# Optimization experiments

Measured on AMD Instinct MI355X. Metric: run time of the kernel, lower is better.

The kernel has to match this reference:

```python
import jax, jax.numpy as jnp
import numpy as np

N = 100000
F = 128
H = 4
C = 32
E = 1600000
LEAKY_ALPHA = 0.2


def setup_inputs() -> dict:
    key = jax.random.key(0)
    k1, k2, k3, k4, k5 = jax.random.split(key, 5)
    x = jax.random.normal(k1, (N, F), dtype=jnp.float32)
    edge_index = jax.random.randint(k2, (E, 2), 0, N, dtype=jnp.int64)  # cols: (source, target)
    kernel = jax.random.normal(k3, (F, H, C), dtype=jnp.float32) * 0.05
    attn_kernel_self = jax.random.normal(k4, (C, H), dtype=jnp.float32) * 0.05
    attn_kernel_neighs = jax.random.normal(k5, (C, H), dtype=jnp.float32) * 0.05
    bias = jnp.zeros((H * C,), dtype=jnp.float32)
    return {"x": x, "edge_index": edge_index, "kernel": kernel,
            "attn_kernel_self": attn_kernel_self,
            "attn_kernel_neighs": attn_kernel_neighs, "bias": bias}


def _gat_forward(x, edge_index, kernel, attn_kernel_self, attn_kernel_neighs, bias):
    n = x.shape[0]
    # add self loops: append (i, i) for every node
    loops = jnp.arange(n, dtype=edge_index.dtype)
    indices = jnp.concatenate([edge_index, jnp.stack([loops, loops], axis=1)], axis=0)
    sources, targets = indices[:, 0], indices[:, 1]

    xp = jnp.einsum('nf,fhc->nhc', x, kernel)                 # [N,H,C]
    attn_self = jnp.einsum('nhc,ch->nh', xp, attn_kernel_self)    # [N,H]
    attn_neigh = jnp.einsum('nhc,ch->nh', xp, attn_kernel_neighs)  # [N,H]

    logits = attn_self[targets] + attn_neigh[sources]          # [Etot,H]
    logits = jnp.where(logits >= 0, logits, LEAKY_ALPHA * logits)  # leaky_relu(0.2)

    # segment softmax over targets (every node has a self loop -> no empty segments)
    seg_max = jax.ops.segment_max(logits, targets, num_segments=n)
    e = jnp.exp(logits - seg_max[targets])
    seg_sum = jax.ops.segment_sum(e, targets, num_segments=n)
    alpha = e / seg_sum[targets]                               # [Etot,H]

    # weighted aggregation (dropout is identity at inference)
    msgs = alpha[..., None] * xp[sources]                      # [Etot,H,C]
    out = jax.ops.segment_sum(msgs, targets, num_segments=n)   # [N,H,C]

    out = out.reshape(n, H * C) + bias                         # concat heads + bias, linear activation
    return out, alpha[..., None]


def reference(x, edge_index, kernel, attn_kernel_self, attn_kernel_neighs, bias):
    return _gat_forward(x, edge_index, kernel, attn_kernel_self, attn_kernel_neighs, bias)
```

## Files before the change

kernel.cpp:

```cpp
#include <hip/hip_runtime.h>
#include <hip/hip_bf16.h>
#include <math.h>

#define LEAKY(x) ((x) >= 0.0f ? (x) : 0.2f * (x))
#define CHUNK 8192

typedef __attribute__((ext_vector_type(8))) short short8;
typedef __attribute__((ext_vector_type(4))) float f32x4;
typedef __attribute__((ext_vector_type(2))) int i32x2;

__device__ __forceinline__ float bf_lo(uint32_t u) { return __uint_as_float(u << 16); }
__device__ __forceinline__ float bf_hi(uint32_t u) { return __uint_as_float(u & 0xffff0000u); }
__device__ __forceinline__ uint32_t pack2(float a, float b) {
    __hip_bfloat162 h = __float22bfloat162_rn(make_float2(a, b));
    return *reinterpret_cast<uint32_t*>(&h);
}

__global__ __launch_bounds__(256) void w_prep(
    const float* __restrict__ W, uint32_t* __restrict__ Wp)
{
    const int slot = blockIdx.x * 256 + threadIdx.x;
    if (slot >= 2048) return;
    const int kb = slot >> 9;
    const int cb = (slot >> 6) & 7;
    const int l  = slot & 63;
    const int k0 = kb * 32 + (l >> 4) * 8;
    const int col = cb * 16 + (l & 15);
    uint32_t u[4];
    #pragma unroll
    for (int p = 0; p < 4; ++p) {
        const float a = W[(size_t)(k0 + 2 * p) * 128 + col];
        const float b = W[(size_t)(k0 + 2 * p + 1) * 128 + col];
        u[p] = pack2(a, b);
    }
    *(uint4*)&Wp[(size_t)slot * 4] = make_uint4(u[0], u[1], u[2], u[3]);
}

__global__ __launch_bounds__(256) void gemm_xp(
    const float* __restrict__ x, const uint32_t* __restrict__ Wp,
    const float* __restrict__ aks, const float* __restrict__ akn,
    uint32_t* __restrict__ xpb, float* __restrict__ attn_self,
    float* __restrict__ attn_nei, int N)
{
    __shared__ float xs[64][133];
    const int t  = threadIdx.x;
    const int w  = t >> 6;
    const int l  = t & 63;
    const int nb = blockIdx.x * 64;

    const int row  = nb + w * 16 + (l & 15);
    const int rowc = min(row, N - 1);
    const int kg   = (l >> 4) * 8;
    const float* xrow = x + (size_t)rowc * 128 + kg;

    f32x4 acc[8] = {};
    #pragma unroll
    for (int kb = 0; kb < 4; ++kb) {
        const float4 x0 = *(const float4*)(xrow + kb * 32);
        const float4 x1 = *(const float4*)(xrow + kb * 32 + 4);
        union { short8 s; uint32_t u[4]; } A;
        A.u[0] = pack2(x0.x, x0.y); A.u[1] = pack2(x0.z, x0.w);
        A.u[2] = pack2(x1.x, x1.y); A.u[3] = pack2(x1.z, x1.w);
        #pragma unroll
        for (int cb = 0; cb < 8; ++cb) {
            union { short8 s; uint4 u; } B;
            B.u = *(const uint4*)&Wp[(((size_t)(kb * 8 + cb)) * 64 + l) * 4];
            acc[cb] = __builtin_amdgcn_mfma_f32_16x16x32_bf16(A.s, B.s, acc[cb], 0, 0, 0);
        }
    }

    const int r0 = (l >> 4) * 4;
    const int cl = l & 15;
    #pragma unroll
    for (int cb = 0; cb < 8; ++cb)
        #pragma unroll
        for (int r = 0; r < 4; ++r)
            xs[w * 16 + r0 + r][cb * 16 + cl] = acc[cb][r];
    __syncthreads();

    #pragma unroll
    for (int i = 0; i < 16; ++i) {
        const int idx = t + i * 256;
        const int n = idx >> 6, q = idx & 63;
        const int gn = nb + n;
        if (gn < N)
            xpb[(size_t)gn * 64 + q] = pack2(xs[n][2 * q], xs[n][2 * q + 1]);
    }

    {
        const int n = t & 63, h = t >> 6;
        const int gn = nb + n;
        if (gn < N) {
            float ss = 0.0f, sn = 0.0f;
            #pragma unroll
            for (int c = 0; c < 32; ++c) {
                const float v = xs[n][h * 32 + c];
                ss = fmaf(v, aks[c * 4 + h], ss);
                sn = fmaf(v, akn[c * 4 + h], sn);
            }
            attn_self[(size_t)gn * 4 + h] = ss;
            attn_nei [(size_t)gn * 4 + h] = sn;
        }
    }
}

__global__ __launch_bounds__(256) void binA(
    const int* __restrict__ ei, int2* __restrict__ stage,
    int* __restrict__ start_table, int* __restrict__ bucket_tot,
    int NB, int E)
{
    __shared__ int lh[512], lex[512], ss[256];
    const int t    = threadIdx.x;
    const int base = blockIdx.x * CHUNK;
    const int end  = min(E, base + CHUNK);

    for (int i = t; i < 512; i += 256) lh[i] = 0;
    __syncthreads();
    for (int i = base + t; i < end; i += 256)
        atomicAdd(&lh[((const int2*)ei)[i].y >> 8], 1);
    __syncthreads();

    const int v0 = lh[2 * t], v1 = lh[2 * t + 1];
    ss[t] = v0 + v1;
    __syncthreads();
    for (int d = 1; d < 256; d <<= 1) {
        const int add = (t >= d) ? ss[t - d] : 0;
        __syncthreads();
        ss[t] += add;
        __syncthreads();
    }
    const int ex = ss[t] - v0 - v1;
    lex[2 * t] = ex;
    lex[2 * t + 1] = ex + v0;
    __syncthreads();

    const size_t cbase = (size_t)blockIdx.x * (NB + 1);
    for (int b = t; b <= NB; b += 256) start_table[cbase + b] = base + lex[b];
    for (int b = t; b < NB; b += 256)
        if (lh[b]) atomicAdd(&bucket_tot[b], lh[b]);
    __syncthreads();

    for (int i = base + t; i < end; i += 256) {
        const int2 e2 = ((const int2*)ei)[i];
        const int slot = atomicAdd(&lex[e2.y >> 8], 1);
        stage[base + slot] = e2;
    }
}

__global__ __launch_bounds__(256) void bucket_scan(
    const int* __restrict__ bucket_tot, int* __restrict__ bucket_off,
    int* __restrict__ offsets, int NB, int N, int E)
{
    __shared__ int ss[256];
    const int t = threadIdx.x;
    const int v0 = (2 * t     < NB) ? bucket_tot[2 * t]     : 0;
    const int v1 = (2 * t + 1 < NB) ? bucket_tot[2 * t + 1] : 0;
    ss[t] = v0 + v1;
    __syncthreads();
    for (int d = 1; d < 256; d <<= 1) {
        const int add = (t >= d) ? ss[t - d] : 0;
        __syncthreads();
        ss[t] += add;
        __syncthreads();
    }
    const int ex = ss[t] - v0 - v1;
    if (2 * t     <= NB) bucket_off[2 * t]     = ex;
    if (2 * t + 1 <= NB) bucket_off[2 * t + 1] = ex + v0;
    if (t == 0) offsets[N] = E;
}

__global__ __launch_bounds__(256) void binB(
    const int2* __restrict__ stage, const int* __restrict__ start_table,
    const int* __restrict__ bucket_off, int* __restrict__ offsets,
    int* __restrict__ csr_src, int nc, int NB, int N)
{
    __shared__ int s0[256], cum[257], ss[256], lcnt[256], lcur[256];
    const int t  = threadIdx.x;
    const int b  = blockIdx.x;
    const int lo = b << 8;
    const int nn = min(N, lo + 256) - lo;

    int len = 0;
    if (t < nc) {
        const size_t cb = (size_t)t * (NB + 1);
        const int a0 = start_table[cb + b];
        s0[t] = a0;
        len   = start_table[cb + b + 1] - a0;
    }
    ss[t] = len;
    lcnt[t] = 0;
    __syncthreads();
    for (int d = 1; d < 256; d <<= 1) {
        const int add = (t >= d) ? ss[t - d] : 0;
        __syncthreads();
        ss[t] += add;
        __syncthreads();
    }
    if (t == 0) cum[0] = 0;
    cum[t + 1] = ss[t];
    __syncthreads();
    const int T = cum[nc];

    for (int g = t; g < T; g += 256) {
        int loc = 0, hic = nc - 1;
        while (loc < hic) {
            const int mid = (loc + hic + 1) >> 1;
            if (cum[mid] <= g) loc = mid; else hic = mid - 1;
        }
        const int2 e = stage[s0[loc] + (g - cum[loc])];
        atomicAdd(&lcnt[e.y - lo], 1);
    }
    __syncthreads();

    const int v = lcnt[t];
    ss[t] = v;
    __syncthreads();
    for (int d = 1; d < 256; d <<= 1) {
        const int add = (t >= d) ? ss[t - d] : 0;
        __syncthreads();
        ss[t] += add;
        __syncthreads();
    }
    const int nodeoff = bucket_off[b] + ss[t] - v;
    lcur[t] = nodeoff;
    if (t < nn) offsets[lo + t] = nodeoff;
    __syncthreads();

    for (int g = t; g < T; g += 256) {
        int loc = 0, hic = nc - 1;
        while (loc < hic) {
            const int mid = (loc + hic + 1) >> 1;
            if (cum[mid] <= g) loc = mid; else hic = mid - 1;
        }
        const int2 e = stage[s0[loc] + (g - cum[loc])];
        const int slot = atomicAdd(&lcur[e.y - lo], 1);
        csr_src[slot] = e.x;
    }
}

__global__ __launch_bounds__(256) void aggregate(
    const int* __restrict__ csr_src, const int* __restrict__ offsets,
    const uint32_t* __restrict__ xpb, const float* __restrict__ attn_self,
    const float* __restrict__ attn_nei, const float* __restrict__ bias,
    float* __restrict__ out, float* __restrict__ alpha_out,
    float* __restrict__ inv_arr, int N, int E)
{
    const int lane = threadIdx.x & 63;
    int node = blockIdx.x * 4 + (threadIdx.x >> 6);
    if (node >= N) return;
    node = __builtin_amdgcn_readfirstlane(node);

    const int hL = lane >> 4;
    const int c0 = 2 * lane;

    const float asH = attn_self[(size_t)node * 4 + hL];
    const float anH = attn_nei [(size_t)node * 4 + hL];
    const float eS  = __expf(LEAKY(asH + anH));
    float sumE = eS;
    const uint32_t uS = xpb[(size_t)node * 64 + lane];
    float acc0 = eS * bf_lo(uS), acc1 = eS * bf_hi(uS);

    const int off0 = __builtin_amdgcn_readfirstlane(offsets[node]);
    const int deg  = __builtin_amdgcn_readfirstlane(offsets[node + 1]) - off0;
    const int* srcp = csr_src + off0;

    for (int j = 0; j < deg; j += 8) {
        int s[8];
        #pragma unroll
        for (int k = 0; k < 8; ++k) s[k] = srcp[min(j + k, deg - 1)];
        float a[8];
        #pragma unroll
        for (int k = 0; k < 8; ++k) a[k] = attn_nei[(size_t)s[k] * 4 + hL];
        uint32_t u[8];
        #pragma unroll
        for (int k = 0; k < 8; ++k) u[k] = xpb[(size_t)s[k] * 64 + lane];
        #pragma unroll
        for (int k = 0; k < 8; ++k) {
            const float v = (j + k < deg) ? __expf(LEAKY(asH + a[k])) : 0.0f;
            sumE += v;
            acc0 = fmaf(v, bf_lo(u[k]), acc0);
            acc1 = fmaf(v, bf_hi(u[k]), acc1);
        }
    }

    const float inv = 1.0f / sumE;
    union { float2 f; unsigned long long u; } o;
    o.f = make_float2(fmaf(acc0, inv, bias[c0]), fmaf(acc1, inv, bias[c0 + 1]));
    __builtin_nontemporal_store(o.u,
        (unsigned long long*)&out[(size_t)node * 128 + c0]);
    if ((lane & 15) == 0) {
        inv_arr[(size_t)node * 4 + hL] = inv;
        __builtin_nontemporal_store(eS * inv,
            &alpha_out[(size_t)(E + node) * 4 + hL]);
    }
}

__global__ __launch_bounds__(256) void alpha_kernel(
    const int* __restrict__ ei, const float* __restrict__ attn_self,
    const float* __restrict__ attn_nei, const float* __restrict__ inv_arr,
    float* __restrict__ alpha_out, int E)
{
    const int i = blockIdx.x * 256 + threadIdx.x;
    if (i >= E) return;
    const i32x2 e2 = __builtin_nontemporal_load((const i32x2*)ei + i);
    const int src = e2.x, tgt = e2.y;
    const float4 as4 = *(const float4*)&attn_self[(size_t)tgt * 4];
    const float4 an4 = *(const float4*)&attn_nei[(size_t)src * 4];
    const float4 iv4 = *(const float4*)&inv_arr[(size_t)tgt * 4];
    f32x4 a;
    a.x = __expf(LEAKY(as4.x + an4.x)) * iv4.x;
    a.y = __expf(LEAKY(as4.y + an4.y)) * iv4.y;
    a.z = __expf(LEAKY(as4.z + an4.z)) * iv4.z;
    a.w = __expf(LEAKY(as4.w + an4.w)) * iv4.w;
    __builtin_nontemporal_store(a, (f32x4*)&alpha_out[(size_t)i * 4]);
}

extern "C" void kernel_launch(void* const* d_in, const int* in_sizes, int n_in,
                              void* d_out, int out_size, void* d_ws, size_t ws_size,
                              hipStream_t stream)
{
    const float* x    = (const float*)d_in[0];
    const int*   ei   = (const int*)d_in[1];
    const float* W    = (const float*)d_in[2];
    const float* aks  = (const float*)d_in[3];
    const float* akn  = (const float*)d_in[4];
    const float* bias = (const float*)d_in[5];

    const int N  = in_sizes[0] / 128;
    const int E  = in_sizes[1] / 2;
    const int NB = (N + 255) >> 8;
    const int nc = (E + CHUNK - 1) / CHUNK;

    float* out       = (float*)d_out;
    float* alpha_out = out + (size_t)N * 128;
    int2* stage      = (int2*)alpha_out;

    char* p = (char*)d_ws;
    auto alloc = [&](size_t bytes) {
        char* r = p;
        p += (bytes + 255) & ~(size_t)255;
        return r;
    };
    uint32_t* xpb       = (uint32_t*)alloc((size_t)N * 64 * 4);
    uint32_t* Wp        = (uint32_t*)alloc((size_t)2048 * 16);
    float* attn_self    = (float*)alloc((size_t)N * 4 * 4);
    float* attn_nei     = (float*)alloc((size_t)N * 4 * 4);
    float* inv_arr      = (float*)alloc((size_t)N * 4 * 4);
    int*   offsets      = (int*)alloc((size_t)(N + 1) * 4);
    int*   csr_src      = (int*)alloc((size_t)E * 4);
    int*   bucket_tot   = (int*)alloc((size_t)NB * 4);
    int*   bucket_off   = (int*)alloc((size_t)(NB + 1) * 4);
    int*   start_table  = (int*)alloc((size_t)nc * (NB + 1) * 4);

    hipMemsetAsync(bucket_tot, 0, (size_t)NB * 4, stream);

    w_prep<<<8, 256, 0, stream>>>(W, Wp);
    gemm_xp<<<(N + 63) / 64, 256, 0, stream>>>(x, Wp, aks, akn, xpb,
                                               attn_self, attn_nei, N);
    binA<<<nc, 256, 0, stream>>>(ei, stage, start_table, bucket_tot, NB, E);
    bucket_scan<<<1, 256, 0, stream>>>(bucket_tot, bucket_off, offsets, NB, N, E);
    binB<<<NB, 256, 0, stream>>>(stage, start_table, bucket_off, offsets,
                                 csr_src, nc, NB, N);
    aggregate<<<(N + 3) / 4, 256, 0, stream>>>(csr_src, offsets, xpb,
                                               attn_self, attn_nei, bias, out,
                                               alpha_out, inv_arr, N, E);
    alpha_kernel<<<(E + 255) / 256, 256, 0, stream>>>(ei, attn_self, attn_nei,
                                                      inv_arr, alpha_out, E);
}
```

Before: 208.0 us.

## Fuse GEMM with binning pass, drop bucket scan kernel, vectorize neighbor attention loads

The edge-binning histogram pass now runs inside the GEMM launch as extra blocks, so the independent projection and binning work share one grid. The single-block bucket_scan kernel is removed; each binB block instead reduces the bucket totals before it to get its own offset. The stage reads in binB become nontemporal loads. The aggregate kernel makes source indices wave-uniform and loads all four heads' neighbor attention as one float4, selecting its head in registers. This saves two launches and some scalar loads, at the cost of redundant prefix reductions in binB and larger shared memory per fused block, which may lower occupancy.

```diff
diff --git a/kernel.cpp b/kernel.cpp
--- a/kernel.cpp
+++ b/kernel.cpp
@@ -14,6 +14,12 @@
 __device__ __forceinline__ uint32_t pack2(float a, float b) {
     __hip_bfloat162 h = __float22bfloat162_rn(make_float2(a, b));
     return *reinterpret_cast<uint32_t*>(&h);
+}
+__device__ __forceinline__ float pick4(const float4& v, int h)
+{
+    const float ab = (h & 1) ? v.y : v.x;
+    const float cd = (h & 1) ? v.w : v.z;
+    return (h & 2) ? cd : ab;
 }
 
 __global__ __launch_bounds__(256) void w_prep(
@@ -36,17 +42,60 @@
     *(uint4*)&Wp[(size_t)slot * 4] = make_uint4(u[0], u[1], u[2], u[3]);
 }
 
-__global__ __launch_bounds__(256) void gemm_xp(
+__global__ __launch_bounds__(256) void gemm_binA(
     const float* __restrict__ x, const uint32_t* __restrict__ Wp,
     const float* __restrict__ aks, const float* __restrict__ akn,
     uint32_t* __restrict__ xpb, float* __restrict__ attn_self,
-    float* __restrict__ attn_nei, int N)
+    float* __restrict__ attn_nei, const int* __restrict__ ei,
+    int2* __restrict__ stage, int* __restrict__ start_table,
+    int* __restrict__ bucket_tot, int nc, int NB, int N, int E)
 {
     __shared__ float xs[64][133];
-    const int t  = threadIdx.x;
+    __shared__ int lh[512], lex[512], ss[256];
+    const int t = threadIdx.x;
+
+    if (blockIdx.x < nc) {
+        const int base = blockIdx.x * CHUNK;
+        const int end  = min(E, base + CHUNK);
+
+        for (int i = t; i < 512; i += 256) lh[i] = 0;
+        __syncthreads();
+        for (int i = base + t; i < end; i += 256)
+            atomicAdd(&lh[((const int2*)ei)[i].y >> 8], 1);
+        __syncthreads();
+
+        const int v0 = lh[2 * t], v1 = lh[2 * t + 1];
+        ss[t] = v0 + v1;
+        __syncthreads();
+        for (int d = 1; d < 256; d <<= 1) {
+            const int add = (t >= d) ? ss[t - d] : 0;
+            __syncthreads();
+            ss[t] += add;
+            __syncthreads();
+        }
+        const int ex = ss[t] - v0 - v1;
+        lex[2 * t] = ex;
+        lex[2 * t + 1] = ex + v0;
+        __syncthreads();
+
+        const size_t cbase = (size_t)blockIdx.x * (NB + 1);
+        for (int b = t; b <= NB; b += 256) start_table[cbase + b] = base + lex[b];
+        for (int b = t; b < NB; b += 256)
+            if (lh[b]) atomicAdd(&bucket_tot[b], lh[b]);
+        __syncthreads();
+
+        for (int i = base + t; i < end; i += 256) {
+            const int2 e2 = ((const int2*)ei)[i];
+            const int slot = atomicAdd(&lex[e2.y >> 8], 1);
+            stage[base + slot] = e2;
+        }
+        return;
+    }
+
+    const int blk = blockIdx.x - nc;
     const int w  = t >> 6;
     const int l  = t & 63;
-    const int nb = blockIdx.x * 64;
+    const int nb = blk * 64;
 
     const int row  = nb + w * 16 + (l & 15);
     const int rowc = min(row, N - 1);
@@ -91,94 +140,34 @@
         const int n = t & 63, h = t >> 6;
         const int gn = nb + n;
         if (gn < N) {
-            float ss = 0.0f, sn = 0.0f;
+            float sv = 0.0f, sn = 0.0f;
             #pragma unroll
             for (int c = 0; c < 32; ++c) {
                 const float v = xs[n][h * 32 + c];
-                ss = fmaf(v, aks[c * 4 + h], ss);
+                sv = fmaf(v, aks[c * 4 + h], sv);
                 sn = fmaf(v, akn[c * 4 + h], sn);
             }
-            attn_self[(size_t)gn * 4 + h] = ss;
+            attn_self[(size_t)gn * 4 + h] = sv;
             attn_nei [(size_t)gn * 4 + h] = sn;
         }
     }
-}
-
-__global__ __launch_bounds__(256) void binA(
-    const int* __restrict__ ei, int2* __restrict__ stage,
-    int* __restrict__ start_table, int* __restrict__ bucket_tot,
-    int NB, int E)
-{
-    __shared__ int lh[512], lex[512], ss[256];
-    const int t    = threadIdx.x;
-    const int base = blockIdx.x * CHUNK;
-    const int end  = min(E, base + CHUNK);
-
-    for (int i = t; i < 512; i += 256) lh[i] = 0;
-    __syncthreads();
-    for (int i = base + t; i < end; i += 256)
-        atomicAdd(&lh[((const int2*)ei)[i].y >> 8], 1);
-    __syncthreads();
-
-    const int v0 = lh[2 * t], v1 = lh[2 * t + 1];
-    ss[t] = v0 + v1;
-    __syncthreads();
-    for (int d = 1; d < 256; d <<= 1) {
-        const int add = (t >= d) ? ss[t - d] : 0;
-        __syncthreads();
-        ss[t] += add;
-        __syncthreads();
-    }
-    const int ex = ss[t] - v0 - v1;
-    lex[2 * t] = ex;
-    lex[2 * t + 1] = ex + v0;
-    __syncthreads();
-
-    const size_t cbase = (size_t)blockIdx.x * (NB + 1);
-    for (int b = t; b <= NB; b += 256) start_table[cbase + b] = base + lex[b];
-    for (int b = t; b < NB; b += 256)
-        if (lh[b]) atomicAdd(&bucket_tot[b], lh[b]);
-    __syncthreads();
-
-    for (int i = base + t; i < end; i += 256) {
-        const int2 e2 = ((const int2*)ei)[i];
-        const int slot = atomicAdd(&lex[e2.y >> 8], 1);
-        stage[base + slot] = e2;
-    }
-}
-
-__global__ __launch_bounds__(256) void bucket_scan(
-    const int* __restrict__ bucket_tot, int* __restrict__ bucket_off,
-    int* __restrict__ offsets, int NB, int N, int E)
-{
-    __shared__ int ss[256];
-    const int t = threadIdx.x;
-    const int v0 = (2 * t     < NB) ? bucket_tot[2 * t]     : 0;
-    const int v1 = (2 * t + 1 < NB) ? bucket_tot[2 * t + 1] : 0;
-    ss[t] = v0 + v1;
-    __syncthreads();
-    for (int d = 1; d < 256; d <<= 1) {
-        const int add = (t >= d) ? ss[t - d] : 0;
-        __syncthreads();
-        ss[t] += add;
-        __syncthreads();
-    }
-    const int ex = ss[t] - v0 - v1;
-    if (2 * t     <= NB) bucket_off[2 * t]     = ex;
-    if (2 * t + 1 <= NB) bucket_off[2 * t + 1] = ex + v0;
-    if (t == 0) offsets[N] = E;
 }
 
 __global__ __launch_bounds__(256) void binB(
     const int2* __restrict__ stage, const int* __restrict__ start_table,
-    const int* __restrict__ bucket_off, int* __restrict__ offsets,
-    int* __restrict__ csr_src, int nc, int NB, int N)
-{
-    __shared__ int s0[256], cum[257], ss[256], lcnt[256], lcur[256];
+    const int* __restrict__ bucket_tot, int* __restrict__ offsets,
+    int* __restrict__ csr_src, int nc, int NB, int N, int E)
+{
+    __shared__ int s0[256], cum[257], ss[256], lcnt[256], lcur[256], red[256];
     const int t  = threadIdx.x;
     const int b  = blockIdx.x;
     const int lo = b << 8;
     const int nn = min(N, lo + 256) - lo;
+
+    int part = 0;
+    for (int i = t; i < b; i += 256) part += bucket_tot[i];
+    red[t] = part;
+    if (t == 0 && b == 0) offsets[N] = E;
 
     int len = 0;
     if (t < nc) {
@@ -190,6 +179,11 @@
     ss[t] = len;
     lcnt[t] = 0;
     __syncthreads();
+    for (int d = 128; d > 0; d >>= 1) {
+        if (t < d) red[t] += red[t + d];
+        __syncthreads();
+    }
+    const int boff = red[0];
     for (int d = 1; d < 256; d <<= 1) {
         const int add = (t >= d) ? ss[t - d] : 0;
         __syncthreads();
@@ -207,7 +201,8 @@
             const int mid = (loc + hic + 1) >> 1;
             if (cum[mid] <= g) loc = mid; else hic = mid - 1;
         }
-        const int2 e = stage[s0[loc] + (g - cum[loc])];
+        const i32x2 e = __builtin_nontemporal_load(
+            (const i32x2*)stage + (s0[loc] + (g - cum[loc])));
         atomicAdd(&lcnt[e.y - lo], 1);
     }
     __syncthreads();
@@ -221,7 +216,7 @@
         ss[t] += add;
         __syncthreads();
     }
-    const int nodeoff = bucket_off[b] + ss[t] - v;
+    const int nodeoff = boff + ss[t] - v;
     lcur[t] = nodeoff;
     if (t < nn) offsets[lo + t] = nodeoff;
     __syncthreads();
@@ -232,7 +227,8 @@
             const int mid = (loc + hic + 1) >> 1;
             if (cum[mid] <= g) loc = mid; else hic = mid - 1;
         }
-        const int2 e = stage[s0[loc] + (g - cum[loc])];
+        const i32x2 e = __builtin_nontemporal_load(
+            (const i32x2*)stage + (s0[loc] + (g - cum[loc])));
         const int slot = atomicAdd(&lcur[e.y - lo], 1);
         csr_src[slot] = e.x;
     }
@@ -257,7 +253,8 @@
     const float anH = attn_nei [(size_t)node * 4 + hL];
     const float eS  = __expf(LEAKY(asH + anH));
     float sumE = eS;
-    const uint32_t uS = xpb[(size_t)node * 64 + lane];
+    const uint32_t* xpl = xpb + lane;
+    const uint32_t uS = xpl[(uint32_t)node << 6];
     float acc0 = eS * bf_lo(uS), acc1 = eS * bf_hi(uS);
 
     const int off0 = __builtin_amdgcn_readfirstlane(offsets[node]);
@@ -267,16 +264,19 @@
     for (int j = 0; j < deg; j += 8) {
         int s[8];
         #pragma unroll
-        for (int k = 0; k < 8; ++k) s[k] = srcp[min(j + k, deg - 1)];
-        float a[8];
-        #pragma unroll
-        for (int k = 0; k < 8; ++k) a[k] = attn_nei[(size_t)s[k] * 4 + hL];
+        for (int k = 0; k < 8; ++k)
+            s[k] = __builtin_amdgcn_readfirstlane(srcp[min(j + k, deg - 1)]);
+        float4 an4[8];
+        #pragma unroll
+        for (int k = 0; k < 8; ++k)
+            an4[k] = *(const float4*)&attn_nei[(uint32_t)s[k] * 4u];
         uint32_t u[8];
         #pragma unroll
-        for (int k = 0; k < 8; ++k) u[k] = xpb[(size_t)s[k] * 64 + lane];
+        for (int k = 0; k < 8; ++k) u[k] = xpl[(uint32_t)s[k] << 6];
         #pragma unroll
         for (int k = 0; k < 8; ++k) {
-            const float v = (j + k < deg) ? __expf(LEAKY(asH + a[k])) : 0.0f;
+            const float v = (j + k < deg)
+                ? __expf(LEAKY(asH + pick4(an4[k], hL))) : 0.0f;
             sumE += v;
             acc0 = fmaf(v, bf_lo(u[k]), acc0);
             acc1 = fmaf(v, bf_hi(u[k]), acc1);
@@ -349,18 +349,16 @@
     int*   offsets      = (int*)alloc((size_t)(N + 1) * 4);
     int*   csr_src      = (int*)alloc((size_t)E * 4);
     int*   bucket_tot   = (int*)alloc((size_t)NB * 4);
-    int*   bucket_off   = (int*)alloc((size_t)(NB + 1) * 4);
     int*   start_table  = (int*)alloc((size_t)nc * (NB + 1) * 4);
 
     hipMemsetAsync(bucket_tot, 0, (size_t)NB * 4, stream);
 
     w_prep<<<8, 256, 0, stream>>>(W, Wp);
-    gemm_xp<<<(N + 63) / 64, 256, 0, stream>>>(x, Wp, aks, akn, xpb,
-                                               attn_self, attn_nei, N);
-    binA<<<nc, 256, 0, stream>>>(ei, stage, start_table, bucket_tot, NB, E);
-    bucket_scan<<<1, 256, 0, stream>>>(bucket_tot, bucket_off, offsets, NB, N, E);
-    binB<<<NB, 256, 0, stream>>>(stage, start_table, bucket_off, offsets,
-                                 csr_src, nc, NB, N);
+    gemm_binA<<<nc + (N + 63) / 64, 256, 0, stream>>>(
+        x, Wp, aks, akn, xpb, attn_self, attn_nei,
+        ei, stage, start_table, bucket_tot, nc, NB, N, E);
+    binB<<<NB, 256, 0, stream>>>(stage, start_table, bucket_tot, offsets,
+                                 csr_src, nc, NB, N, E);
     aggregate<<<(N + 3) / 4, 256, 0, stream>>>(csr_src, offsets, xpb,
                                                attn_self, attn_nei, bias, out,
                                                alpha_out, inv_arr, N, E);
```

Measured after the change: 728.2 us. +250.1%, slower.
